# Optimization experiments

Measured on AMD Instinct MI355X. Metric: run time of the kernel, lower is better.

Reference implementation:

```python
import jax, jax.numpy as jnp
import numpy as np

TOPK = 16  # matches selected per (frame, query pixel)


def setup_inputs() -> dict:
    key = jax.random.key(0)
    ks = jax.random.split(key, 4)
    B, T, N, C = 2, 3, 4096, 256  # batch, ref frames, 64x64 tokens, channels
    scale = 1.0 / np.sqrt(C)
    return {
        "tgt": jax.random.normal(ks[0], (B, N, C), dtype=jnp.float32),
        "ref": jax.random.normal(ks[1], (B, T, N, C), dtype=jnp.float32),
        "Wq": jax.random.normal(ks[2], (C, C), dtype=jnp.float32) * scale,
        "bq": jnp.zeros((C,), dtype=jnp.float32),
        "Wk": jax.random.normal(ks[3], (C, C), dtype=jnp.float32) * scale,
        "bk": jnp.zeros((C,), dtype=jnp.float32),
    }


def _l2norm(x, eps=1e-12):
    return x * jax.lax.rsqrt(jnp.sum(x * x, axis=-1, keepdims=True) + eps)


def reference(tgt, ref, Wq, bq, Wk, bk):
    # tgt: [B, Nq, C] target-frame tokens; ref: [B, T, Nr, C] reference-frame tokens
    B, Nq, C = tgt.shape
    T, Nr = ref.shape[1], ref.shape[2]
    q = _l2norm(tgt @ Wq + bq)                      # [B, Nq, C]
    k = _l2norm(ref @ Wk + bk)                      # [B, T, Nr, C]
    # cross-frame cosine-similarity correlation volume
    sim = jnp.einsum("bqc,btrc->btqr", q, k)        # [B, T, Nq, Nr]
    # top-k matched reference locations per query pixel
    topv, topi = jax.lax.top_k(sim, TOPK)           # [B, T, Nq, K]
    # gather matched reference features (irregular gather)
    bi = jnp.arange(B)[:, None, None, None]
    ti = jnp.arange(T)[None, :, None, None]
    gathered = ref[bi, ti, topi]                    # [B, T, Nq, K, C]
    # attention-weighted aggregation of matched features
    w = jax.nn.softmax(topv, axis=-1)               # [B, T, Nq, K]
    out = jnp.einsum("btqk,btqkc->btqc", w, gathered)  # [B, T, Nq, C]
    return out
```

## Files before the change

### kernel.cpp

```cpp
#include <hip/hip_runtime.h>
#include <hip/hip_fp16.h>
#include <stdint.h>

#define T_FRAMES 3
#define NTOK 4096
#define CH 256

typedef __attribute__((ext_vector_type(8))) short bf16x8;
typedef __attribute__((ext_vector_type(4))) float f32x4;
typedef __attribute__((address_space(1))) void gvoid;
typedef __attribute__((address_space(3))) void svoid;

__device__ __forceinline__ unsigned short f2bf_rne(float f) {
  union { float f; uint32_t u; } c; c.f = f;
  uint32_t u = c.u;
  return (unsigned short)((u + 0x7FFFu + ((u >> 16) & 1u)) >> 16);
}
__device__ __forceinline__ float bflo(uint32_t x) { return __uint_as_float(x << 16); }
__device__ __forceinline__ float bfhi(uint32_t x) { return __uint_as_float(x & 0xFFFF0000u); }

__global__ __launch_bounds__(256) void proj_kernel(
    const float* __restrict__ Xq, const float* __restrict__ Wq, const float* __restrict__ bq,
    const float* __restrict__ Xk, const float* __restrict__ Wk, const float* __restrict__ bk,
    unsigned short* __restrict__ Qb, float* __restrict__ Qlo,
    unsigned short* __restrict__ Kb, float* __restrict__ Klo)
{
  __shared__ double At[64][32];
  const int tid = threadIdx.x;
  int blk = blockIdx.x;
  const float *X, *W, *bias; unsigned short* Pb; float* Plo;
  if (blk < 256) { X = Xq; W = Wq; bias = bq; Pb = Qb; Plo = Qlo; }
  else           { X = Xk; W = Wk; bias = bk; Pb = Kb; Plo = Klo; blk -= 256; }
  const int rbase = blk * 32;
  const int wv = tid >> 6, lane = tid & 63;
  const int r0 = wv * 8;
  const int c4 = lane * 4;

  double acc[8][4];
  #pragma unroll
  for (int i = 0; i < 8; i++) {
    #pragma unroll
    for (int j = 0; j < 4; j++) acc[i][j] = (double)bias[c4 + j];
  }

  const int srow = tid & 31, skq = (tid >> 5) * 8;
  for (int kc = 0; kc < CH; kc += 64) {
    {
      const float* xp = X + (size_t)(rbase + srow) * CH + kc + skq;
      const float4 v0 = *(const float4*)(xp);
      const float4 v1 = *(const float4*)(xp + 4);
      At[skq + 0][srow] = (double)v0.x; At[skq + 1][srow] = (double)v0.y;
      At[skq + 2][srow] = (double)v0.z; At[skq + 3][srow] = (double)v0.w;
      At[skq + 4][srow] = (double)v1.x; At[skq + 5][srow] = (double)v1.y;
      At[skq + 6][srow] = (double)v1.z; At[skq + 7][srow] = (double)v1.w;
    }
    __syncthreads();
    #pragma unroll 8
    for (int k = 0; k < 64; k++) {
      const float4 w4 = *(const float4*)(W + (size_t)(kc + k) * CH + c4);
      const double b0 = (double)w4.x, b1 = (double)w4.y;
      const double b2 = (double)w4.z, b3 = (double)w4.w;
      double a[8];
      #pragma unroll
      for (int i = 0; i < 4; i++) {
        const double2 ap = *(const double2*)&At[k][r0 + 2 * i];
        a[2*i] = ap.x; a[2*i+1] = ap.y;
      }
      #pragma unroll
      for (int i = 0; i < 8; i++) {
        acc[i][0] += a[i] * b0; acc[i][1] += a[i] * b1;
        acc[i][2] += a[i] * b2; acc[i][3] += a[i] * b3;
      }
    }
    __syncthreads();
  }

  #pragma unroll
  for (int i = 0; i < 8; i++) {
    double ss = acc[i][0]*acc[i][0] + acc[i][1]*acc[i][1]
              + acc[i][2]*acc[i][2] + acc[i][3]*acc[i][3];
    #pragma unroll
    for (int off = 32; off >= 1; off >>= 1) ss += __shfl_xor(ss, off);
    const double inv = 1.0 / sqrt(ss + 1e-12);
    const size_t base = (size_t)(rbase + r0 + i) * CH + c4;
    double vd[4]; float fb[4]; unsigned short us[4];
    #pragma unroll
    for (int j = 0; j < 4; j++) {
      vd[j] = acc[i][j] * inv;
      us[j] = f2bf_rne((float)vd[j]);
      fb[j] = __uint_as_float(((uint32_t)us[j]) << 16);
    }
    uint2 pk; pk.x = (uint32_t)us[0] | ((uint32_t)us[1] << 16);
    pk.y = (uint32_t)us[2] | ((uint32_t)us[3] << 16);
    *(uint2*)(Pb + base) = pk;
    float4 lo;
    lo.x = (float)(vd[0] - (double)fb[0]); lo.y = (float)(vd[1] - (double)fb[1]);
    lo.z = (float)(vd[2] - (double)fb[2]); lo.w = (float)(vd[3] - (double)fb[3]);
    *(float4*)(Plo + base) = lo;
  }
}

__global__ __launch_bounds__(256) void ref16_kernel(
    const float* __restrict__ ref, unsigned short* __restrict__ ref16)
{
  const size_t i = ((size_t)blockIdx.x * 256 + threadIdx.x) * 8;
  const float4 v0 = *(const float4*)(ref + i);
  const float4 v1 = *(const float4*)(ref + i + 4);
  const uint32_t h0 = (uint32_t)__half_as_ushort(__float2half_rn(v0.x));
  const uint32_t h1 = (uint32_t)__half_as_ushort(__float2half_rn(v0.y));
  const uint32_t h2 = (uint32_t)__half_as_ushort(__float2half_rn(v0.z));
  const uint32_t h3 = (uint32_t)__half_as_ushort(__float2half_rn(v0.w));
  const uint32_t h4 = (uint32_t)__half_as_ushort(__float2half_rn(v1.x));
  const uint32_t h5 = (uint32_t)__half_as_ushort(__float2half_rn(v1.y));
  const uint32_t h6 = (uint32_t)__half_as_ushort(__float2half_rn(v1.z));
  const uint32_t h7 = (uint32_t)__half_as_ushort(__float2half_rn(v1.w));
  uint4 hv;
  hv.x = h0 | (h1 << 16); hv.y = h2 | (h3 << 16);
  hv.z = h4 | (h5 << 16); hv.w = h6 | (h7 << 16);
  *(uint4*)(ref16 + i) = hv;
}

__global__ __launch_bounds__(256, 4) void sim_cand_kernel(
    const unsigned short* __restrict__ Qb,
    const unsigned short* __restrict__ Kb,
    uint32_t* __restrict__ cand)
{
  __shared__ unsigned short kst[2][32 * 256];
  const int bid = blockIdx.x;
  const int rs = bid & 3;
  const int qb = (bid >> 2) & 63;
  const int bt = bid >> 8;
  const int b = bt / T_FRAMES;
  const int tid = threadIdx.x;
  const int wv = tid >> 6, lane = tid & 63;
  const int lq = lane & 15, g = lane >> 4;
  const int q = qb * 64 + wv * 16 + lq;

  bf16x8 bfr[8];
  {
    const unsigned short* qrow = Qb + (size_t)(b * NTOK + q) * CH + g * 8;
    #pragma unroll
    for (int kc = 0; kc < 8; kc++) bfr[kc] = *(const bf16x8*)(qrow + kc * 32);
  }
  uint32_t best[16];
  #pragma unroll
  for (int i = 0; i < 16; i++) best[i] = 0u;
  uint32_t s[16];

  const unsigned short* kbase = Kb + ((size_t)bt * NTOK + (size_t)rs * 1024) * CH;

#define STAGE(C, BUFI)                                                          \
  {                                                                             \
    _Pragma("unroll")                                                           \
    for (int t = 0; t < 4; t++) {                                               \
      const int o16 = (wv * 4 + t) * 64 + lane;                                 \
      const int row = o16 >> 5, colp = o16 & 31;                                \
      const int col16 = (colp - row) & 31;                                      \
      const unsigned short* gsrc = kbase + (size_t)((C) * 32 + row) * CH + col16 * 8; \
      __builtin_amdgcn_global_load_lds((const gvoid*)gsrc,                      \
          (svoid*)(&kst[BUFI][0] + (size_t)(wv * 4 + t) * 512), 16, 0, 0);      \
    }                                                                           \
  }

#define COMPUTE_HALF(CBASE, BUFI, SOFF)                                         \
  {                                                                             \
    _Pragma("unroll")                                                           \
    for (int t = 0; t < 2; t++) {                                               \
      f32x4 acc = {2.0f, 2.0f, 2.0f, 2.0f};                                     \
      const int arow = t * 16 + lq;                                             \
      const unsigned short* rowp = &kst[BUFI][0] + (size_t)arow * 256;          \
      _Pragma("unroll")                                                         \
      for (int kc = 0; kc < 8; kc++) {                                          \
        const int colp = (kc * 4 + g + arow) & 31;                              \
        const bf16x8 a = *(const bf16x8*)(rowp + colp * 8);                     \
        acc = __builtin_amdgcn_mfma_f32_16x16x32_bf16(a, bfr[kc], acc, 0, 0, 0);\
      }                                                                         \
      _Pragma("unroll")                                                         \
      for (int j = 0; j < 4; j++) {                                             \
        const uint32_t bits = __float_as_uint(acc[j]);                          \
        s[(SOFF) + t * 4 + j] = (bits & 0xFFFFFC00u) |                          \
            (uint32_t)((CBASE) * 32 + t * 16 + g * 4 + j);                      \
      }                                                                         \
    }                                                                           \
  }

#define SORT16_MERGE()                                                          \
  {                                                                             \
    _Pragma("unroll")                                                           \
    for (int bk = 2; bk <= 16; bk <<= 1) {                                      \
      _Pragma("unroll")                                                         \
      for (int bj = bk >> 1; bj > 0; bj >>= 1) {                                \
        _Pragma("unroll")                                                       \
        for (int i = 0; i < 16; i++) {                                          \
          const int l = i ^ bj;                                                 \
          if (l > i) {                                                          \
            const bool up = ((i & bk) != 0);                                    \
            const uint32_t a2 = s[i], b2 = s[l];                                \
            const uint32_t mn = a2 < b2 ? a2 : b2;                              \
            const uint32_t mx = a2 < b2 ? b2 : a2;                              \
            s[i] = up ? mn : mx; s[l] = up ? mx : mn;                           \
          }                                                                     \
        }                                                                       \
      }                                                                         \
    }                                                                           \
    uint32_t m[16];                                                             \
    _Pragma("unroll")                                                           \
    for (int i = 0; i < 16; i++) {                                              \
      const uint32_t a2 = best[i], b2 = s[15 - i];                              \
      m[i] = a2 > b2 ? a2 : b2;                                                 \
    }                                                                           \
    _Pragma("unroll")                                                           \
    for (int bj = 8; bj > 0; bj >>= 1) {                                        \
      _Pragma("unroll")                                                         \
      for (int i = 0; i < 16; i++) {                                            \
        const int l = i ^ bj;                                                   \
        if (l > i) {                                                            \
          const uint32_t a2 = m[i], b2 = m[l];                                  \
          const uint32_t mn = a2 < b2 ? a2 : b2;                                \
          const uint32_t mx = a2 < b2 ? b2 : a2;                                \
          m[i] = mx; m[l] = mn;                                                 \
        }                                                                       \
      }                                                                         \
    }                                                                           \
    _Pragma("unroll")                                                           \
    for (int i = 0; i < 16; i++) best[i] = m[i];                                \
  }

  STAGE(0, 0);
  __syncthreads();
  for (int cp = 0; cp < 16; cp++) {
    const int c0 = 2 * cp;
    STAGE(c0 + 1, 1);
    COMPUTE_HALF(c0, 0, 0);
    __syncthreads();
    if (cp < 15) STAGE(c0 + 2, 0);
    COMPUTE_HALF(c0 + 1, 1, 8);
    SORT16_MERGE();
    __syncthreads();
  }

  #pragma unroll
  for (int st = 16; st <= 32; st <<= 1) {
    uint32_t o[16];
    #pragma unroll
    for (int i = 0; i < 16; i++) o[i] = (uint32_t)__shfl_xor((int)best[15 - i], st);
    #pragma unroll
    for (int i = 0; i < 16; i++) best[i] = best[i] > o[i] ? best[i] : o[i];
    #pragma unroll
    for (int bj = 8; bj > 0; bj >>= 1) {
      #pragma unroll
      for (int i = 0; i < 16; i++) {
        const int l = i ^ bj;
        if (l > i) {
          const uint32_t a2 = best[i], b2 = best[l];
          const uint32_t mn = a2 < b2 ? a2 : b2;
          const uint32_t mx = a2 < b2 ? b2 : a2;
          best[i] = mx; best[l] = mn;
        }
      }
    }
  }
  if (g == 0) {
    uint32_t* cp2 = cand + ((size_t)bt * NTOK + q) * 64 + rs * 16;
    #pragma unroll
    for (int i = 0; i < 16; i += 4) {
      uint4 v; v.x = best[i]; v.y = best[i+1]; v.z = best[i+2]; v.w = best[i+3];
      *(uint4*)(cp2 + i) = v;
    }
  }
#undef STAGE
#undef COMPUTE_HALF
#undef SORT16_MERGE
}

__global__ __launch_bounds__(256) void out_kernel(
    const unsigned short* __restrict__ Qb, const float* __restrict__ Qlo,
    const unsigned short* __restrict__ Kb, const float* __restrict__ Klo,
    const uint32_t* __restrict__ cand, const float* __restrict__ ref,
    const unsigned short* __restrict__ ref16, int use16,
    float* __restrict__ out)
{
  const int tid = threadIdx.x, wv = tid >> 6, lane = tid & 63;
  const int bid = blockIdx.x;
  const int work = (bid & 7) * 768 + (bid >> 3);
  const int rowid = work * 4 + wv;
  const int bt = rowid >> 12, q = rowid & 4095;
  const int b = bt / T_FRAMES;

  const uint32_t k0 = cand[(size_t)rowid * 64 + lane];
  uint32_t key = (k0 & 0xFFFFF000u) | ((uint32_t)(lane >> 4) << 10) | (k0 & 0x3FFu);

  #pragma unroll
  for (int k = 2; k <= 64; k <<= 1) {
    #pragma unroll
    for (int j = k >> 1; j > 0; j >>= 1) {
      const uint32_t ok = (uint32_t)__shfl_xor((int)key, j);
      const bool takeMax = (((lane & j) != 0) == ((lane & k) == 0));
      if ((ok > key) == takeMax) key = ok;
    }
  }
  const float v = __uint_as_float(key & 0xFFFFF000u) - 2.0f;
  int rr = (int)(key & 0xFFFu);

  const float v16c = __shfl(v, 48);
  const float BW = 4.5e-3f;
  const bool band = fabsf(v - v16c) <= BW;

  const uint2 qbv = *(const uint2*)(Qb + (size_t)(b * NTOK + q) * CH + lane * 4);
  const float4 qlv = *(const float4*)(Qlo + (size_t)(b * NTOK + q) * CH + lane * 4);
  const double qd0 = (double)bflo(qbv.x) + (double)qlv.x;
  const double qd1 = (double)bfhi(qbv.x) + (double)qlv.y;
  const double qd2 = (double)bflo(qbv.y) + (double)qlv.z;
  const double qd3 = (double)bfhi(qbv.y) + (double)qlv.w;

  const unsigned short* kbp = Kb + (size_t)bt * NTOK * CH;
  const float* klp = Klo + (size_t)bt * NTOK * CH;

  double dval = -1.0e300;
  {
    const unsigned long long bm = __ballot(band);
    const int lo = __ffsll(bm) - 1;
    const int hi = 63 - __clzll(bm);
    for (int idx = lo; idx <= hi; idx++) {
      const int ri = __shfl(rr, idx);
      const uint2 kbv = *(const uint2*)(kbp + (size_t)ri * CH + lane * 4);
      const float4 klv = *(const float4*)(klp + (size_t)ri * CH + lane * 4);
      double dd = qd0 * ((double)bflo(kbv.x) + (double)klv.x)
                + qd1 * ((double)bfhi(kbv.x) + (double)klv.y)
                + qd2 * ((double)bflo(kbv.y) + (double)klv.z)
                + qd3 * ((double)bfhi(kbv.y) + (double)klv.w);
      #pragma unroll
      for (int off = 32; off >= 1; off >>= 1) dd += __shfl_xor(dd, off);
      if (lane == idx) dval = dd;
    }
  }
  double p = band ? dval : ((v > v16c + BW) ? (double)v : -1.0e300);

  #pragma unroll
  for (int k = 2; k <= 64; k <<= 1) {
    #pragma unroll
    for (int j = k >> 1; j > 0; j >>= 1) {
      const double op = __shfl_xor(p, j);
      const int orr = __shfl_xor(rr, j);
      const bool takeMax = (((lane & j) != 0) == ((lane & k) == 0));
      const bool og = (op > p) || (op == p && orr < rr);
      if (takeMax == og) { p = op; rr = orr; }
    }
  }

  double pm = p;
  #pragma unroll
  for (int j = 8; j >= 1; j >>= 1) pm = fmax(pm, __shfl_xor(pm, j));
  double e = (lane >= 48) ? exp(p - pm) : 0.0;
  double es = e;
  #pragma unroll
  for (int j = 8; j >= 1; j >>= 1) es += __shfl_xor(es, j);
  const float w = (float)(e / es);

  float a0 = 0.f, a1 = 0.f, a2 = 0.f, a3 = 0.f;
  if (use16) {
    const unsigned short* rb16 = ref16 + (size_t)bt * NTOK * CH + lane * 4;
    #pragma unroll
    for (int i = 0; i < 16; i++) {
      const float wi = __shfl(w, 48 + i);
      const int ri = __shfl(rr, 48 + i) & 0xFFF;
      const uint2 hv = *(const uint2*)(rb16 + (size_t)ri * CH);
      a0 += wi * __half2float(__ushort_as_half((unsigned short)(hv.x & 0xFFFFu)));
      a1 += wi * __half2float(__ushort_as_half((unsigned short)(hv.x >> 16)));
      a2 += wi * __half2float(__ushort_as_half((unsigned short)(hv.y & 0xFFFFu)));
      a3 += wi * __half2float(__ushort_as_half((unsigned short)(hv.y >> 16)));
    }
  } else {
    const float* rbp = ref + (size_t)bt * NTOK * CH + lane * 4;
    #pragma unroll
    for (int i = 0; i < 16; i++) {
      const float wi = __shfl(w, 48 + i);
      const int ri = __shfl(rr, 48 + i) & 0xFFF;
      const float4 f = *(const float4*)(rbp + (size_t)ri * CH);
      a0 += wi * f.x; a1 += wi * f.y; a2 += wi * f.z; a3 += wi * f.w;
    }
  }
  float4 o; o.x = a0; o.y = a1; o.z = a2; o.w = a3;
  *(float4*)(out + (size_t)rowid * CH + lane * 4) = o;
}

extern "C" void kernel_launch(void* const* d_in, const int* in_sizes, int n_in,
                              void* d_out, int out_size, void* d_ws, size_t ws_size,
                              hipStream_t stream) {
  const float* tgt = (const float*)d_in[0];
  const float* ref = (const float*)d_in[1];
  const float* Wq  = (const float*)d_in[2];
  const float* bq  = (const float*)d_in[3];
  const float* Wk  = (const float*)d_in[4];
  const float* bk  = (const float*)d_in[5];
  float* out = (float*)d_out;

  const int B = 2;
  const int RQ = B * NTOK;
  const int RK = B * T_FRAMES * NTOK;

  char* ws = (char*)d_ws;
  unsigned short* Qb = (unsigned short*)ws; ws += (size_t)RQ * CH * 2;
  float* Qlo = (float*)ws;                  ws += (size_t)RQ * CH * 4;
  unsigned short* Kb = (unsigned short*)ws; ws += (size_t)RK * CH * 2;
  float* Klo = (float*)ws;                  ws += (size_t)RK * CH * 4;
  uint32_t* cand = (uint32_t*)ws;           ws += (size_t)RK * 64 * 4;
  const bool big = ws_size >= (size_t)69206016;
  unsigned short* ref16 = big ? (unsigned short*)ws : nullptr;
  const int use16 = big ? 1 : 0;

  proj_kernel<<<RQ / 32 + RK / 32, 256, 0, stream>>>(
      tgt, Wq, bq, ref, Wk, bk, Qb, Qlo, Kb, Klo);
  if (big) ref16_kernel<<<3072, 256, 0, stream>>>(ref, ref16);
  sim_cand_kernel<<<6 * 64 * 4, 256, 0, stream>>>(Qb, Kb, cand);
  out_kernel<<<RK / 4, 256, 0, stream>>>(Qb, Qlo, Kb, Klo, cand, ref, ref16, use16, out);
}
```

Before: 264.7 us.

## Split projection K dimension across two thread halves with 16-row tiles

The fp64 projection kernel now uses 512-thread blocks over 16-row tiles, loading the full 256-wide input slice into shared memory once. Each half of the block accumulates over half of the K dimension, and the partial sums are combined through shared memory before normalisation. This doubles the number of blocks and halves the per-thread accumulator count, aiming at more parallelism and occupancy for the fp64 FMA work. The cost is an extra shared-memory reduction step, and each weight row is now read by twice as many blocks.

Result: slower. 277.8 us (+4.9%).

```diff
diff --git a/kernel.cpp b/kernel.cpp
--- a/kernel.cpp
+++ b/kernel.cpp
@@ -19,84 +19,101 @@
 __device__ __forceinline__ float bflo(uint32_t x) { return __uint_as_float(x << 16); }
 __device__ __forceinline__ float bfhi(uint32_t x) { return __uint_as_float(x & 0xFFFF0000u); }
 
-__global__ __launch_bounds__(256) void proj_kernel(
+__global__ __launch_bounds__(512) void proj_kernel(
     const float* __restrict__ Xq, const float* __restrict__ Wq, const float* __restrict__ bq,
     const float* __restrict__ Xk, const float* __restrict__ Wk, const float* __restrict__ bk,
     unsigned short* __restrict__ Qb, float* __restrict__ Qlo,
     unsigned short* __restrict__ Kb, float* __restrict__ Klo)
 {
-  __shared__ double At[64][32];
+  __shared__ double At[256][16];
   const int tid = threadIdx.x;
   int blk = blockIdx.x;
   const float *X, *W, *bias; unsigned short* Pb; float* Plo;
-  if (blk < 256) { X = Xq; W = Wq; bias = bq; Pb = Qb; Plo = Qlo; }
-  else           { X = Xk; W = Wk; bias = bk; Pb = Kb; Plo = Klo; blk -= 256; }
-  const int rbase = blk * 32;
-  const int wv = tid >> 6, lane = tid & 63;
-  const int r0 = wv * 8;
-  const int c4 = lane * 4;
-
-  double acc[8][4];
-  #pragma unroll
-  for (int i = 0; i < 8; i++) {
-    #pragma unroll
-    for (int j = 0; j < 4; j++) acc[i][j] = (double)bias[c4 + j];
-  }
-
-  const int srow = tid & 31, skq = (tid >> 5) * 8;
-  for (int kc = 0; kc < CH; kc += 64) {
-    {
-      const float* xp = X + (size_t)(rbase + srow) * CH + kc + skq;
-      const float4 v0 = *(const float4*)(xp);
-      const float4 v1 = *(const float4*)(xp + 4);
-      At[skq + 0][srow] = (double)v0.x; At[skq + 1][srow] = (double)v0.y;
-      At[skq + 2][srow] = (double)v0.z; At[skq + 3][srow] = (double)v0.w;
-      At[skq + 4][srow] = (double)v1.x; At[skq + 5][srow] = (double)v1.y;
-      At[skq + 6][srow] = (double)v1.z; At[skq + 7][srow] = (double)v1.w;
-    }
-    __syncthreads();
-    #pragma unroll 8
-    for (int k = 0; k < 64; k++) {
-      const float4 w4 = *(const float4*)(W + (size_t)(kc + k) * CH + c4);
-      const double b0 = (double)w4.x, b1 = (double)w4.y;
-      const double b2 = (double)w4.z, b3 = (double)w4.w;
-      double a[8];
-      #pragma unroll
-      for (int i = 0; i < 4; i++) {
-        const double2 ap = *(const double2*)&At[k][r0 + 2 * i];
-        a[2*i] = ap.x; a[2*i+1] = ap.y;
+  if (blk < 512) { X = Xq; W = Wq; bias = bq; Pb = Qb; Plo = Qlo; }
+  else           { X = Xk; W = Wk; bias = bk; Pb = Kb; Plo = Klo; blk -= 512; }
+  const int rbase = blk * 16;
+  const int kh = tid >> 8;
+  const int t8 = tid & 255;
+  const int r0 = (t8 >> 6) * 4;
+  const int c4 = (t8 & 63) * 4;
+
+  {
+    const int srow = tid & 15, skq = (tid >> 4) * 8;
+    const float* xp = X + (size_t)(rbase + srow) * CH + skq;
+    const float4 v0 = *(const float4*)(xp);
+    const float4 v1 = *(const float4*)(xp + 4);
+    At[skq + 0][srow] = (double)v0.x; At[skq + 1][srow] = (double)v0.y;
+    At[skq + 2][srow] = (double)v0.z; At[skq + 3][srow] = (double)v0.w;
+    At[skq + 4][srow] = (double)v1.x; At[skq + 5][srow] = (double)v1.y;
+    At[skq + 6][srow] = (double)v1.z; At[skq + 7][srow] = (double)v1.w;
+  }
+
+  double acc[4][4];
+  #pragma unroll
+  for (int i = 0; i < 4; i++) {
+    #pragma unroll
+    for (int j = 0; j < 4; j++) acc[i][j] = kh ? 0.0 : (double)bias[c4 + j];
+  }
+  __syncthreads();
+
+  const int k0 = kh * 128;
+  #pragma unroll 4
+  for (int k = k0; k < k0 + 128; k++) {
+    const float4 w4 = *(const float4*)(W + (size_t)k * CH + c4);
+    const double b0 = (double)w4.x, b1 = (double)w4.y;
+    const double b2 = (double)w4.z, b3 = (double)w4.w;
+    double a[4];
+    #pragma unroll
+    for (int i = 0; i < 2; i++) {
+      const double2 ap = *(const double2*)&At[k][r0 + 2 * i];
+      a[2*i] = ap.x; a[2*i+1] = ap.y;
+    }
+    #pragma unroll
+    for (int i = 0; i < 4; i++) {
+      acc[i][0] += a[i] * b0; acc[i][1] += a[i] * b1;
+      acc[i][2] += a[i] * b2; acc[i][3] += a[i] * b3;
+    }
+  }
+
+  __syncthreads();
+  double* ex = &At[0][0];
+  if (kh) {
+    #pragma unroll
+    for (int i = 0; i < 4; i++) {
+      #pragma unroll
+      for (int j = 0; j < 4; j++) ex[(i * 4 + j) * 256 + t8] = acc[i][j];
+    }
+  }
+  __syncthreads();
+  if (!kh) {
+    #pragma unroll
+    for (int i = 0; i < 4; i++) {
+      #pragma unroll
+      for (int j = 0; j < 4; j++) acc[i][j] += ex[(i * 4 + j) * 256 + t8];
+    }
+    #pragma unroll
+    for (int i = 0; i < 4; i++) {
+      double ss = acc[i][0]*acc[i][0] + acc[i][1]*acc[i][1]
+                + acc[i][2]*acc[i][2] + acc[i][3]*acc[i][3];
+      #pragma unroll
+      for (int off = 32; off >= 1; off >>= 1) ss += __shfl_xor(ss, off);
+      const double inv = 1.0 / sqrt(ss + 1e-12);
+      const size_t base = (size_t)(rbase + r0 + i) * CH + c4;
+      double vd[4]; float fb[4]; unsigned short us[4];
+      #pragma unroll
+      for (int j = 0; j < 4; j++) {
+        vd[j] = acc[i][j] * inv;
+        us[j] = f2bf_rne((float)vd[j]);
+        fb[j] = __uint_as_float(((uint32_t)us[j]) << 16);
       }
-      #pragma unroll
-      for (int i = 0; i < 8; i++) {
-        acc[i][0] += a[i] * b0; acc[i][1] += a[i] * b1;
-        acc[i][2] += a[i] * b2; acc[i][3] += a[i] * b3;
-      }
-    }
-    __syncthreads();
-  }
-
-  #pragma unroll
-  for (int i = 0; i < 8; i++) {
-    double ss = acc[i][0]*acc[i][0] + acc[i][1]*acc[i][1]
-              + acc[i][2]*acc[i][2] + acc[i][3]*acc[i][3];
-    #pragma unroll
-    for (int off = 32; off >= 1; off >>= 1) ss += __shfl_xor(ss, off);
-    const double inv = 1.0 / sqrt(ss + 1e-12);
-    const size_t base = (size_t)(rbase + r0 + i) * CH + c4;
-    double vd[4]; float fb[4]; unsigned short us[4];
-    #pragma unroll
-    for (int j = 0; j < 4; j++) {
-      vd[j] = acc[i][j] * inv;
-      us[j] = f2bf_rne((float)vd[j]);
-      fb[j] = __uint_as_float(((uint32_t)us[j]) << 16);
-    }
-    uint2 pk; pk.x = (uint32_t)us[0] | ((uint32_t)us[1] << 16);
-    pk.y = (uint32_t)us[2] | ((uint32_t)us[3] << 16);
-    *(uint2*)(Pb + base) = pk;
-    float4 lo;
-    lo.x = (float)(vd[0] - (double)fb[0]); lo.y = (float)(vd[1] - (double)fb[1]);
-    lo.z = (float)(vd[2] - (double)fb[2]); lo.w = (float)(vd[3] - (double)fb[3]);
-    *(float4*)(Plo + base) = lo;
+      uint2 pk; pk.x = (uint32_t)us[0] | ((uint32_t)us[1] << 16);
+      pk.y = (uint32_t)us[2] | ((uint32_t)us[3] << 16);
+      *(uint2*)(Pb + base) = pk;
+      float4 lo;
+      lo.x = (float)(vd[0] - (double)fb[0]); lo.y = (float)(vd[1] - (double)fb[1]);
+      lo.z = (float)(vd[2] - (double)fb[2]); lo.w = (float)(vd[3] - (double)fb[3]);
+      *(float4*)(Plo + base) = lo;
+    }
   }
 }
 
@@ -409,7 +426,7 @@
   unsigned short* ref16 = big ? (unsigned short*)ws : nullptr;
   const int use16 = big ? 1 : 0;
 
-  proj_kernel<<<RQ / 32 + RK / 32, 256, 0, stream>>>(
+  proj_kernel<<<RQ / 16 + RK / 16, 512, 0, stream>>>(
       tgt, Wq, bq, ref, Wk, bk, Qb, Qlo, Kb, Klo);
   if (big) ref16_kernel<<<3072, 256, 0, stream>>>(ref, ref16);
   sim_cand_kernel<<<6 * 64 * 4, 256, 0, stream>>>(Qb, Kb, cand);
```
